# Kernel optimization log

Hardware: AMD Instinct MI355X
Metric: run time of the kernel (lower is better)

## Reference

```python
import jax, jax.numpy as jnp
import numpy as np

B, HRES, WRES, C, HEADS, WS, SS = 32, 64, 64, 256, 8, 8, 4
N = WS * WS
HID = 4 * C
EPS = 1e-5


def _rel_pos_index(ws):
    coords = np.stack(np.meshgrid(np.arange(ws), np.arange(ws), indexing='ij'))  # [2,ws,ws]
    cf = coords.reshape(2, -1)
    rel = (cf[:, :, None] - cf[:, None, :]).transpose(1, 2, 0)  # [N,N,2]
    rel[:, :, 0] += ws - 1
    rel[:, :, 1] += ws - 1
    rel[:, :, 0] *= 2 * ws - 1
    return rel.sum(-1).reshape(-1)  # [N*N]


def _attn_mask(H, W, ws, ss):
    img = np.zeros((H, W))
    cnt = 0
    for hs in (slice(0, -ws), slice(-ws, -ss), slice(-ss, None)):
        for wsl in (slice(0, -ws), slice(-ws, -ss), slice(-ss, None)):
            img[hs, wsl] = cnt
            cnt += 1
    mw = img.reshape(H // ws, ws, W // ws, ws).transpose(0, 2, 1, 3).reshape(-1, ws * ws)
    am = mw[:, None, :] - mw[:, :, None]  # [nW,N,N]
    return np.where(am != 0, -100.0, 0.0).astype(np.float32)


_RPI = jnp.asarray(_rel_pos_index(WS))
_MASK = jnp.asarray(_attn_mask(HRES, WRES, WS, SS))  # [nW,N,N]


def _ln(x, g, b):
    m = x.mean(-1, keepdims=True)
    v = ((x - m) ** 2).mean(-1, keepdims=True)
    return (x - m) / jnp.sqrt(v + EPS) * g + b


def setup_inputs() -> dict:
    key = jax.random.key(0)
    ks = jax.random.split(key, 16)
    s = 0.02
    return {
        'x': jax.random.normal(ks[0], (B, HRES * WRES, C), jnp.float32),
        'norm1_g': jnp.ones((C,), jnp.float32),
        'norm1_b': jnp.zeros((C,), jnp.float32),
        'qkv_w': jax.random.normal(ks[1], (3 * C, C), jnp.float32) * s,
        'qkv_b': jnp.zeros((3 * C,), jnp.float32),
        'rpb_table': jax.random.normal(ks[2], ((2 * WS - 1) ** 2, HEADS), jnp.float32) * s,
        'proj_w': jax.random.normal(ks[3], (C, C), jnp.float32) * s,
        'proj_b': jnp.zeros((C,), jnp.float32),
        'norm2_g': jnp.ones((C,), jnp.float32),
        'norm2_b': jnp.zeros((C,), jnp.float32),
        'fc1_w': jax.random.normal(ks[4], (HID, C), jnp.float32) * s,
        'fc1_b': jnp.zeros((HID,), jnp.float32),
        'fc2_w': jax.random.normal(ks[5], (C, HID), jnp.float32) * s,
        'fc2_b': jnp.zeros((C,), jnp.float32),
        'H': HRES,
        'W': WRES,
    }


def reference(x, norm1_g, norm1_b, qkv_w, qkv_b, rpb_table, proj_w, proj_b,
              norm2_g, norm2_b, fc1_w, fc1_b, fc2_w, fc2_b, H, W):
    Bn, L, Cd = x.shape
    ws, ss, nh = WS, SS, HEADS
    hd = Cd // nh
    shortcut = x
    h = _ln(x, norm1_g, norm1_b).reshape(Bn, H, W, Cd)
    # cyclic shift (H,W divisible by ws -> no padding needed)
    h = jnp.roll(h, (-ss, -ss), axis=(1, 2))
    # window partition: [B,H,W,C] -> [B*nW, N, C]
    h = h.reshape(Bn, H // ws, ws, W // ws, ws, Cd).transpose(0, 1, 3, 2, 4, 5).reshape(-1, N, Cd)
    qkv = (h @ qkv_w.T + qkv_b).reshape(-1, N, 3, nh, hd).transpose(2, 0, 3, 1, 4)
    q, k, v = qkv[0], qkv[1], qkv[2]  # [B_,h,N,d]
    attn = jnp.einsum('bhnd,bhmd->bhnm', q * (hd ** -0.5), k)
    rpb = rpb_table[_RPI].reshape(N, N, nh).transpose(2, 0, 1)  # [h,N,N]
    attn = attn + rpb[None]
    nW = _MASK.shape[0]
    attn = attn.reshape(Bn, nW, nh, N, N) + _MASK[None, :, None]
    attn = jax.nn.softmax(attn.reshape(-1, nh, N, N), axis=-1)
    o = jnp.einsum('bhnm,bhmd->bhnd', attn, v).transpose(0, 2, 1, 3).reshape(-1, N, Cd)
    o = o @ proj_w.T + proj_b
    # window reverse + reverse shift
    o = o.reshape(Bn, H // ws, W // ws, ws, ws, Cd).transpose(0, 1, 3, 2, 4, 5).reshape(Bn, H, W, Cd)
    o = jnp.roll(o, (ss, ss), axis=(1, 2)).reshape(Bn, L, Cd)
    x = shortcut + o
    h2 = _ln(x, norm2_g, norm2_b)
    h2 = jax.nn.gelu(h2 @ fc1_w.T + fc1_b, approximate=False)
    return x + (h2 @ fc2_w.T + fc2_b)
```

## Files before the change

kernel.cpp:

```cpp
#include <hip/hip_runtime.h>
#include <hip/hip_bf16.h>
#include <stdint.h>

typedef __bf16 bf16_t;
typedef __bf16 bf16x8 __attribute__((ext_vector_type(8)));
typedef __bf16 bf16x4 __attribute__((ext_vector_type(4)));
typedef float f32x4 __attribute__((ext_vector_type(4)));

#define MROWS 131072

__device__ __forceinline__ bf16_t to_bf16(float f) {
  __hip_bfloat16 h = __float2bfloat16(f);
  return *reinterpret_cast<bf16_t*>(&h);
}

__device__ __forceinline__ f32x4 mfma16(bf16x8 a, bf16x8 b, f32x4 c) {
  return __builtin_amdgcn_mfma_f32_16x16x32_bf16(a, b, c, 0, 0, 0);
}

__device__ __forceinline__ void gload16(const void* g, void* l) {
  __builtin_amdgcn_global_load_lds(
      (const __attribute__((address_space(1))) void*)g,
      (__attribute__((address_space(3))) void*)l, 16, 0, 0);
}

__device__ __forceinline__ int map_row(int m) {
  int b   = m >> 12;
  int rem = m & 4095;
  int win = rem >> 6;
  int n   = rem & 63;
  int gh  = ((win >> 3) << 3) + (n >> 3);
  int gw  = ((win & 7) << 3) + (n & 7);
  int sh  = (gh + 4) & 63;
  int sw  = (gw + 4) & 63;
  return (b << 12) + (sh << 6) + sw;
}

__global__ __launch_bounds__(256) void cvt_kernel(const float* __restrict__ in,
                                                  bf16_t* __restrict__ out, int n) {
  int i = blockIdx.x * 256 + threadIdx.x;
  if (i < n) out[i] = to_bf16(in[i]);
}

__global__ __launch_bounds__(256) void bias_kernel(const float* __restrict__ rpbt,
                                                   float* __restrict__ bias) {
  int idx = blockIdx.x * 256 + threadIdx.x;
  int m = idx & 63, n = (idx >> 6) & 63, h = (idx >> 12) & 7, c = idx >> 15;
  int yn = n >> 3, xn = n & 7, ym = m >> 3, xm = m & 7;
  float v = rpbt[((yn - ym + 7) * 15 + (xn - xm + 7)) * 8 + h];
  int rn = (c & 2) ? (yn < 4 ? 1 : 2) : 0;
  int cn = (c & 1) ? (xn < 4 ? 1 : 2) : 0;
  int rm = (c & 2) ? (ym < 4 ? 1 : 2) : 0;
  int cm = (c & 1) ? (xm < 4 ? 1 : 2) : 0;
  if (rn * 3 + cn != rm * 3 + cm) v -= 100.0f;
  bias[idx] = v;
}

template <bool PERM>
__global__ __launch_bounds__(256) void ln_kernel(const float* __restrict__ xin,
                                                 const float* __restrict__ g,
                                                 const float* __restrict__ b,
                                                 bf16_t* __restrict__ out) {
  int row  = (blockIdx.x << 2) + (threadIdx.x >> 6);
  int lane = threadIdx.x & 63;
  int src  = PERM ? map_row(row) : row;
  float4 v = *reinterpret_cast<const float4*>(xin + (size_t)src * 256 + (lane << 2));
  float s = v.x + v.y + v.z + v.w;
#pragma unroll
  for (int d = 1; d < 64; d <<= 1) s += __shfl_xor(s, d);
  float mean = s * 0.00390625f;
  float ax = v.x - mean, ay = v.y - mean, az = v.z - mean, aw = v.w - mean;
  float s2 = ax * ax + ay * ay + az * az + aw * aw;
#pragma unroll
  for (int d = 1; d < 64; d <<= 1) s2 += __shfl_xor(s2, d);
  float rstd = rsqrtf(s2 * 0.00390625f + 1e-5f);
  float4 gv = *reinterpret_cast<const float4*>(g + (lane << 2));
  float4 bv = *reinterpret_cast<const float4*>(b + (lane << 2));
  bf16x4 o4;
  o4[0] = to_bf16(ax * rstd * gv.x + bv.x);
  o4[1] = to_bf16(ay * rstd * gv.y + bv.y);
  o4[2] = to_bf16(az * rstd * gv.z + bv.z);
  o4[3] = to_bf16(aw * rstd * gv.w + bv.w);
  *reinterpret_cast<bf16x4*>(out + (size_t)row * 256 + (lane << 2)) = o4;
}

template <int EPI>
__global__ __launch_bounds__(256) void gemm_bt(const bf16_t* __restrict__ A,
                                               const bf16_t* __restrict__ W,
                                               const float* __restrict__ bias,
                                               void* __restrict__ outp,
                                               void* __restrict__ outp2,
                                               void* __restrict__ outp3,
                                               const float* __restrict__ resid,
                                               int M, int N, int K) {
  __shared__ __align__(16) bf16_t As[128 * 32];
  __shared__ __align__(16) bf16_t Bs[128 * 32];
  const int tid  = threadIdx.x;
  const int lane = tid & 63, lo = lane & 15, hi = lane >> 4;
  const int wave = tid >> 6;
  const int bm = blockIdx.x << 7, bn = blockIdx.y << 7;
  const int wr = (wave >> 1) << 6, wc = (wave & 1) << 6;
  f32x4 acc[4][4] = {};

  for (int k0 = 0; k0 < K; k0 += 32) {
    __syncthreads();
#pragma unroll
    for (int it = 0; it < 2; ++it) {
      int ch = (it << 8) + tid;
      int r = ch >> 2, kf = (ch & 3) << 3;
      gload16(A + (size_t)(bm + r) * K + (k0 + kf), &As[ch << 3]);
      gload16(W + (size_t)(bn + r) * K + (k0 + kf), &Bs[ch << 3]);
    }
    __syncthreads();
    bf16x8 af[4], bfr[4];
#pragma unroll
    for (int i = 0; i < 4; ++i)
      af[i] = *reinterpret_cast<const bf16x8*>(&As[(wr + (i << 4) + lo) * 32 + (hi << 3)]);
#pragma unroll
    for (int j = 0; j < 4; ++j)
      bfr[j] = *reinterpret_cast<const bf16x8*>(&Bs[(wc + (j << 4) + lo) * 32 + (hi << 3)]);
#pragma unroll
    for (int i = 0; i < 4; ++i)
#pragma unroll
      for (int j = 0; j < 4; ++j)
        acc[i][j] = mfma16(af[i], bfr[j], acc[i][j]);
  }

  float bv[4];
#pragma unroll
  for (int j = 0; j < 4; ++j) bv[j] = bias[bn + wc + (j << 4) + lo];

#pragma unroll
  for (int i = 0; i < 4; ++i) {
#pragma unroll
    for (int r = 0; r < 4; ++r) {
      int row = bm + wr + (i << 4) + (hi << 2) + r;
      if constexpr (EPI == 2) {
        int xr = map_row(row);
        float* o = (float*)outp;
#pragma unroll
        for (int j = 0; j < 4; ++j) {
          int col = bn + wc + (j << 4) + lo;
          size_t idx = (size_t)xr * 256 + col;
          o[idx] = resid[idx] + acc[i][j][r] + bv[j];
        }
      } else if constexpr (EPI == 3) {
        float* o = (float*)outp;
#pragma unroll
        for (int j = 0; j < 4; ++j) {
          int col = bn + wc + (j << 4) + lo;
          size_t idx = (size_t)row * 256 + col;
          o[idx] = o[idx] + acc[i][j][r] + bv[j];
        }
      } else if constexpr (EPI == 4) {
#pragma unroll
        for (int j = 0; j < 4; ++j) {
          int col = bn + wc + (j << 4) + lo;
          bf16_t* base = (col < 256) ? (bf16_t*)outp
                        : (col < 512) ? (bf16_t*)outp2 : (bf16_t*)outp3;
          int hd = (col >> 5) & 7, d = col & 31;
          base[((size_t)hd * MROWS + row) * 32 + d] = to_bf16(acc[i][j][r] + bv[j]);
        }
      } else {
        bf16_t* o = (bf16_t*)outp;
#pragma unroll
        for (int j = 0; j < 4; ++j) {
          int col = bn + wc + (j << 4) + lo;
          float v = acc[i][j][r] + bv[j];
          if constexpr (EPI == 1) v = 0.5f * v * (1.0f + erff(v * 0.70710678118654752f));
          o[(size_t)row * N + col] = to_bf16(v);
        }
      }
    }
  }
}

__global__ __launch_bounds__(256) void attn_kernel(const bf16_t* __restrict__ qh,
                                                   const bf16_t* __restrict__ kh,
                                                   const bf16_t* __restrict__ vh,
                                                   const float* __restrict__ bias,
                                                   bf16_t* __restrict__ o) {
  __shared__ __align__(16) bf16_t Pl[4][64 * 72];
  __shared__ __align__(16) bf16_t Vt[4][32 * 72];
  const int wave = threadIdx.x >> 6, lane = threadIdx.x & 63;
  const int lo = lane & 15, hi = lane >> 4;
  const int id = (blockIdx.x << 2) + wave;
  const int win = id >> 3, h = id & 7;
  const size_t hb = ((size_t)h * MROWS + (size_t)win * 64) * 32;
  const bf16_t* qb = qh + hb;
  const bf16_t* kb = kh + hb;
  const bf16_t* vb = vh + hb;

  const bf16_t* vbl = vb + lane * 32;
#pragma unroll
  for (int c4 = 0; c4 < 4; ++c4) {
    bf16x8 v8 = *reinterpret_cast<const bf16x8*>(vbl + (c4 << 3));
#pragma unroll
    for (int e = 0; e < 8; ++e) Vt[wave][((c4 << 3) + e) * 72 + lane] = v8[e];
  }

  bf16x8 qa[4], ka[4];
#pragma unroll
  for (int i = 0; i < 4; ++i)
    qa[i] = *reinterpret_cast<const bf16x8*>(qb + ((i << 4) + lo) * 32 + (hi << 3));
#pragma unroll
  for (int j = 0; j < 4; ++j)
    ka[j] = *reinterpret_cast<const bf16x8*>(kb + ((j << 4) + lo) * 32 + (hi << 3));
  f32x4 s[4][4] = {};
#pragma unroll
  for (int i = 0; i < 4; ++i)
#pragma unroll
    for (int j = 0; j < 4; ++j) s[i][j] = mfma16(qa[i], ka[j], s[i][j]);

  const int wh = (win & 63) >> 3, ww = win & 7;
  const int cls = ((wh == 7) ? 2 : 0) + ((ww == 7) ? 1 : 0);
  const float* bb = bias + ((size_t)cls * 8 + h) * 4096;
  const float scale = 0.17677669529663687f;

  float pinv[4][4];
#pragma unroll
  for (int i = 0; i < 4; ++i) {
#pragma unroll
    for (int r = 0; r < 4; ++r) {
      int n = (i << 4) + (hi << 2) + r;
      const float* brow = bb + n * 64 + lo;
      float vals[4], mx = -1e30f;
#pragma unroll
      for (int j = 0; j < 4; ++j) {
        float val = s[i][j][r] * scale + brow[j << 4];
        vals[j] = val;
        mx = fmaxf(mx, val);
      }
#pragma unroll
      for (int d = 1; d < 16; d <<= 1) mx = fmaxf(mx, __shfl_xor(mx, d));
      float sum = 0.0f;
#pragma unroll
      for (int j = 0; j < 4; ++j) {
        float p = __expf(vals[j] - mx);
        sum += p;
        Pl[wave][n * 72 + (j << 4) + lo] = to_bf16(p);
      }
#pragma unroll
      for (int d = 1; d < 16; d <<= 1) sum += __shfl_xor(sum, d);
      pinv[i][r] = 1.0f / sum;
    }
  }

  __syncthreads();

  f32x4 oa[4][2] = {};
#pragma unroll
  for (int kt = 0; kt < 2; ++kt) {
    bf16x8 pa[4], va[2];
#pragma unroll
    for (int i = 0; i < 4; ++i)
      pa[i] = *reinterpret_cast<const bf16x8*>(&Pl[wave][((i << 4) + lo) * 72 + (kt << 5) + (hi << 3)]);
#pragma unroll
    for (int dt = 0; dt < 2; ++dt)
      va[dt] = *reinterpret_cast<const bf16x8*>(&Vt[wave][((dt << 4) + lo) * 72 + (kt << 5) + (hi << 3)]);
#pragma unroll
    for (int i = 0; i < 4; ++i)
#pragma unroll
      for (int dt = 0; dt < 2; ++dt) oa[i][dt] = mfma16(pa[i], va[dt], oa[i][dt]);
  }

  bf16_t* ob = o + (size_t)win * (64 * 256) + h * 32;
#pragma unroll
  for (int i = 0; i < 4; ++i)
#pragma unroll
    for (int r = 0; r < 4; ++r) {
      int n = (i << 4) + (hi << 2) + r;
      float piv = pinv[i][r];
#pragma unroll
      for (int dt = 0; dt < 2; ++dt)
        ob[(size_t)n * 256 + (dt << 4) + lo] = to_bf16(oa[i][dt][r] * piv);
    }
}

extern "C" void kernel_launch(void* const* d_in, const int* in_sizes, int n_in,
                              void* d_out, int out_size, void* d_ws, size_t ws_size,
                              hipStream_t stream) {
  const float* x      = (const float*)d_in[0];
  const float* n1g    = (const float*)d_in[1];
  const float* n1b    = (const float*)d_in[2];
  const float* qkv_w  = (const float*)d_in[3];
  const float* qkv_b  = (const float*)d_in[4];
  const float* rpbt   = (const float*)d_in[5];
  const float* proj_w = (const float*)d_in[6];
  const float* proj_b = (const float*)d_in[7];
  const float* n2g    = (const float*)d_in[8];
  const float* n2b    = (const float*)d_in[9];
  const float* fc1_w  = (const float*)d_in[10];
  const float* fc1_b  = (const float*)d_in[11];
  const float* fc2_w  = (const float*)d_in[12];
  const float* fc2_b  = (const float*)d_in[13];
  float* out = (float*)d_out;
  char*  ws  = (char*)d_ws;

  const size_t MB64 = 67108864;
  bf16_t* hln  = (bf16_t*)(ws);
  bf16_t* obuf = (bf16_t*)(ws);
  bf16_t* h2   = (bf16_t*)(ws);
  bf16_t* qbuf = (bf16_t*)(ws + MB64);
  bf16_t* x2n  = (bf16_t*)(ws + MB64);
  bf16_t* wb   = (bf16_t*)(ws + 2 * MB64);
  bf16_t* qkv_wb  = wb;
  bf16_t* proj_wb = qkv_wb + 196608;
  bf16_t* fc1_wb  = proj_wb + 65536;
  bf16_t* fc2_wb  = fc1_wb + 262144;
  float*  biast   = (float*)(fc2_wb + 262144);
  bf16_t* kbuf = (bf16_t*)d_out;
  bf16_t* vbuf = kbuf + 33554432;

  cvt_kernel<<<768, 256, 0, stream>>>(qkv_w, qkv_wb, 196608);
  cvt_kernel<<<256, 256, 0, stream>>>(proj_w, proj_wb, 65536);
  cvt_kernel<<<1024, 256, 0, stream>>>(fc1_w, fc1_wb, 262144);
  cvt_kernel<<<1024, 256, 0, stream>>>(fc2_w, fc2_wb, 262144);
  bias_kernel<<<512, 256, 0, stream>>>(rpbt, biast);

  ln_kernel<true><<<32768, 256, 0, stream>>>(x, n1g, n1b, hln);

  gemm_bt<4><<<dim3(1024, 6), 256, 0, stream>>>(hln, qkv_wb, qkv_b, qbuf, kbuf, vbuf,
                                                nullptr, MROWS, 768, 256);

  attn_kernel<<<4096, 256, 0, stream>>>(qbuf, kbuf, vbuf, biast, obuf);

  gemm_bt<2><<<dim3(1024, 2), 256, 0, stream>>>(obuf, proj_wb, proj_b, out, nullptr, nullptr,
                                                x, MROWS, 256, 256);

  ln_kernel<false><<<32768, 256, 0, stream>>>(out, n2g, n2b, x2n);

  for (int c = 0; c < 4; ++c) {
    const bf16_t* xa = x2n + (size_t)c * 32768 * 256;
    gemm_bt<1><<<dim3(256, 8), 256, 0, stream>>>(xa, fc1_wb, fc1_b, h2, nullptr, nullptr,
                                                 nullptr, 32768, 1024, 256);
    gemm_bt<3><<<dim3(256, 2), 256, 0, stream>>>(h2, fc2_wb, fc2_b, out + (size_t)c * 32768 * 256,
                                                 nullptr, nullptr, nullptr, 32768, 256, 1024);
  }
}
```

Measured before the change: 681.4 us.

## Fuse LN1, QKV projection, window attention and output projection into one kernel

Replaces the separate LN1, QKV GEMM, attention and proj GEMM kernels with a single per-window kernel. Each block takes one window, with one wave per head, and keeps the normalized rows, q/k/v and the attention output in LDS. This removes the round trips of the intermediate QKV and attention-output tensors through global memory. Weights are now read straight from global memory per wave without LDS tiling, and the large LDS footprint limits occupancy. The MLP GEMM grid is also swapped so blockIdx.x walks the N tiles.

Result: faster. 644.4 us (-5.4%).

```diff
diff --git a/kernel.cpp b/kernel.cpp
--- a/kernel.cpp
+++ b/kernel.cpp
@@ -4,7 +4,6 @@
 
 typedef __bf16 bf16_t;
 typedef __bf16 bf16x8 __attribute__((ext_vector_type(8)));
-typedef __bf16 bf16x4 __attribute__((ext_vector_type(4)));
 typedef float f32x4 __attribute__((ext_vector_type(4)));
 
 #define MROWS 131072
@@ -56,15 +55,13 @@
   bias[idx] = v;
 }
 
-template <bool PERM>
 __global__ __launch_bounds__(256) void ln_kernel(const float* __restrict__ xin,
                                                  const float* __restrict__ g,
                                                  const float* __restrict__ b,
                                                  bf16_t* __restrict__ out) {
   int row  = (blockIdx.x << 2) + (threadIdx.x >> 6);
   int lane = threadIdx.x & 63;
-  int src  = PERM ? map_row(row) : row;
-  float4 v = *reinterpret_cast<const float4*>(xin + (size_t)src * 256 + (lane << 2));
+  float4 v = *reinterpret_cast<const float4*>(xin + (size_t)row * 256 + (lane << 2));
   float s = v.x + v.y + v.z + v.w;
 #pragma unroll
   for (int d = 1; d < 64; d <<= 1) s += __shfl_xor(s, d);
@@ -76,6 +73,7 @@
   float rstd = rsqrtf(s2 * 0.00390625f + 1e-5f);
   float4 gv = *reinterpret_cast<const float4*>(g + (lane << 2));
   float4 bv = *reinterpret_cast<const float4*>(b + (lane << 2));
+  typedef __bf16 bf16x4 __attribute__((ext_vector_type(4)));
   bf16x4 o4;
   o4[0] = to_bf16(ax * rstd * gv.x + bv.x);
   o4[1] = to_bf16(ay * rstd * gv.y + bv.y);
@@ -89,16 +87,13 @@
                                                const bf16_t* __restrict__ W,
                                                const float* __restrict__ bias,
                                                void* __restrict__ outp,
-                                               void* __restrict__ outp2,
-                                               void* __restrict__ outp3,
-                                               const float* __restrict__ resid,
                                                int M, int N, int K) {
   __shared__ __align__(16) bf16_t As[128 * 32];
   __shared__ __align__(16) bf16_t Bs[128 * 32];
   const int tid  = threadIdx.x;
   const int lane = tid & 63, lo = lane & 15, hi = lane >> 4;
   const int wave = tid >> 6;
-  const int bm = blockIdx.x << 7, bn = blockIdx.y << 7;
+  const int bm = blockIdx.y << 7, bn = blockIdx.x << 7;
   const int wr = (wave >> 1) << 6, wc = (wave & 1) << 6;
   f32x4 acc[4][4] = {};
 
@@ -135,31 +130,13 @@
 #pragma unroll
     for (int r = 0; r < 4; ++r) {
       int row = bm + wr + (i << 4) + (hi << 2) + r;
-      if constexpr (EPI == 2) {
-        int xr = map_row(row);
-        float* o = (float*)outp;
-#pragma unroll
-        for (int j = 0; j < 4; ++j) {
-          int col = bn + wc + (j << 4) + lo;
-          size_t idx = (size_t)xr * 256 + col;
-          o[idx] = resid[idx] + acc[i][j][r] + bv[j];
-        }
-      } else if constexpr (EPI == 3) {
+      if constexpr (EPI == 3) {
         float* o = (float*)outp;
 #pragma unroll
         for (int j = 0; j < 4; ++j) {
           int col = bn + wc + (j << 4) + lo;
           size_t idx = (size_t)row * 256 + col;
           o[idx] = o[idx] + acc[i][j][r] + bv[j];
-        }
-      } else if constexpr (EPI == 4) {
-#pragma unroll
-        for (int j = 0; j < 4; ++j) {
-          int col = bn + wc + (j << 4) + lo;
-          bf16_t* base = (col < 256) ? (bf16_t*)outp
-                        : (col < 512) ? (bf16_t*)outp2 : (bf16_t*)outp3;
-          int hd = (col >> 5) & 7, d = col & 31;
-          base[((size_t)hd * MROWS + row) * 32 + d] = to_bf16(acc[i][j][r] + bv[j]);
         }
       } else {
         bf16_t* o = (bf16_t*)outp;
@@ -175,42 +152,117 @@
   }
 }
 
-__global__ __launch_bounds__(256) void attn_kernel(const bf16_t* __restrict__ qh,
-                                                   const bf16_t* __restrict__ kh,
-                                                   const bf16_t* __restrict__ vh,
-                                                   const float* __restrict__ bias,
-                                                   bf16_t* __restrict__ o) {
-  __shared__ __align__(16) bf16_t Pl[4][64 * 72];
-  __shared__ __align__(16) bf16_t Vt[4][32 * 72];
-  const int wave = threadIdx.x >> 6, lane = threadIdx.x & 63;
-  const int lo = lane & 15, hi = lane >> 4;
-  const int id = (blockIdx.x << 2) + wave;
-  const int win = id >> 3, h = id & 7;
-  const size_t hb = ((size_t)h * MROWS + (size_t)win * 64) * 32;
-  const bf16_t* qb = qh + hb;
-  const bf16_t* kb = kh + hb;
-  const bf16_t* vb = vh + hb;
-
-  const bf16_t* vbl = vb + lane * 32;
-#pragma unroll
-  for (int c4 = 0; c4 < 4; ++c4) {
-    bf16x8 v8 = *reinterpret_cast<const bf16x8*>(vbl + (c4 << 3));
-#pragma unroll
-    for (int e = 0; e < 8; ++e) Vt[wave][((c4 << 3) + e) * 72 + lane] = v8[e];
-  }
+__global__ __launch_bounds__(512, 2) void mega_attn(
+    const float* __restrict__ x, const float* __restrict__ n1g,
+    const float* __restrict__ n1b, const bf16_t* __restrict__ qkv_wb,
+    const float* __restrict__ qkv_b, const bf16_t* __restrict__ proj_wb,
+    const float* __restrict__ proj_b, const float* __restrict__ bias,
+    float* __restrict__ out) {
+  extern __shared__ __align__(16) char smem_raw[];
+  bf16_t* Sm = (bf16_t*)smem_raw;
+  bf16_t* A_lds = Sm;
+  const int tid = threadIdx.x;
+  const int lane = tid & 63, lo = lane & 15, hi = lane >> 4;
+  const int h = tid >> 6;
+  const int win = blockIdx.x;
+  bf16_t* Wv    = Sm + 16896 + h * 7424;
+  bf16_t* q_lds = Wv;
+  bf16_t* k_lds = Wv + 2560;
+  bf16_t* Vt    = Wv + 5120;
+  bf16_t* Pl    = Wv;
+
+  {
+    const int row = tid >> 3, s = tid & 7;
+    const int src = map_row((win << 6) + row);
+    const float* xp = x + (size_t)src * 256 + (s << 5);
+    float f[32];
+#pragma unroll
+    for (int c = 0; c < 8; ++c) {
+      float4 v = *reinterpret_cast<const float4*>(xp + (c << 2));
+      f[c * 4 + 0] = v.x; f[c * 4 + 1] = v.y; f[c * 4 + 2] = v.z; f[c * 4 + 3] = v.w;
+    }
+    float sum = 0.0f;
+#pragma unroll
+    for (int e = 0; e < 32; ++e) sum += f[e];
+#pragma unroll
+    for (int d = 1; d < 8; d <<= 1) sum += __shfl_xor(sum, d);
+    float mean = sum * 0.00390625f;
+    float var = 0.0f;
+#pragma unroll
+    for (int e = 0; e < 32; ++e) { float t = f[e] - mean; var += t * t; }
+#pragma unroll
+    for (int d = 1; d < 8; d <<= 1) var += __shfl_xor(var, d);
+    float rstd = rsqrtf(var * 0.00390625f + 1e-5f);
+    const float* gp = n1g + (s << 5);
+    const float* bp = n1b + (s << 5);
+#pragma unroll
+    for (int c = 0; c < 4; ++c) {
+      bf16x8 w;
+#pragma unroll
+      for (int e = 0; e < 8; ++e) {
+        int idx = (c << 3) + e;
+        w[e] = to_bf16((f[idx] - mean) * rstd * gp[idx] + bp[idx]);
+      }
+      *reinterpret_cast<bf16x8*>(&A_lds[row * 264 + (s << 5) + (c << 3)]) = w;
+    }
+  }
+  __syncthreads();
+
+  f32x4 aq[2][4] = {}, ak[2][4] = {}, av[2][4] = {};
+#pragma unroll 2
+  for (int kk = 0; kk < 8; ++kk) {
+    const int k0 = kk << 5;
+    bf16x8 fb[4];
+#pragma unroll
+    for (int j = 0; j < 4; ++j)
+      fb[j] = *reinterpret_cast<const bf16x8*>(&A_lds[((j << 4) + lo) * 264 + k0 + (hi << 3)]);
+    bf16x8 wfq[2], wfk[2], wfv[2];
+#pragma unroll
+    for (int i = 0; i < 2; ++i) {
+      int drow = h * 32 + (i << 4) + lo;
+      wfq[i] = *reinterpret_cast<const bf16x8*>(qkv_wb + (size_t)(drow      ) * 256 + k0 + (hi << 3));
+      wfk[i] = *reinterpret_cast<const bf16x8*>(qkv_wb + (size_t)(drow + 256) * 256 + k0 + (hi << 3));
+      wfv[i] = *reinterpret_cast<const bf16x8*>(qkv_wb + (size_t)(drow + 512) * 256 + k0 + (hi << 3));
+    }
+#pragma unroll
+    for (int i = 0; i < 2; ++i)
+#pragma unroll
+      for (int j = 0; j < 4; ++j) {
+        aq[i][j] = mfma16(wfq[i], fb[j], aq[i][j]);
+        ak[i][j] = mfma16(wfk[i], fb[j], ak[i][j]);
+        av[i][j] = mfma16(wfv[i], fb[j], av[i][j]);
+      }
+  }
+
+#pragma unroll
+  for (int i = 0; i < 2; ++i)
+#pragma unroll
+    for (int r = 0; r < 4; ++r) {
+      int d = (i << 4) + (hi << 2) + r;
+      float bq = qkv_b[h * 32 + d];
+      float bk = qkv_b[256 + h * 32 + d];
+      float bv = qkv_b[512 + h * 32 + d];
+#pragma unroll
+      for (int j = 0; j < 4; ++j) {
+        int n = (j << 4) + lo;
+        q_lds[n * 40 + d] = to_bf16(aq[i][j][r] + bq);
+        k_lds[n * 40 + d] = to_bf16(ak[i][j][r] + bk);
+        Vt[d * 72 + n]    = to_bf16(av[i][j][r] + bv);
+      }
+    }
 
   bf16x8 qa[4], ka[4];
 #pragma unroll
   for (int i = 0; i < 4; ++i)
-    qa[i] = *reinterpret_cast<const bf16x8*>(qb + ((i << 4) + lo) * 32 + (hi << 3));
+    qa[i] = *reinterpret_cast<const bf16x8*>(&q_lds[((i << 4) + lo) * 40 + (hi << 3)]);
 #pragma unroll
   for (int j = 0; j < 4; ++j)
-    ka[j] = *reinterpret_cast<const bf16x8*>(kb + ((j << 4) + lo) * 32 + (hi << 3));
-  f32x4 s[4][4] = {};
+    ka[j] = *reinterpret_cast<const bf16x8*>(&k_lds[((j << 4) + lo) * 40 + (hi << 3)]);
+  f32x4 s4[4][4] = {};
 #pragma unroll
   for (int i = 0; i < 4; ++i)
 #pragma unroll
-    for (int j = 0; j < 4; ++j) s[i][j] = mfma16(qa[i], ka[j], s[i][j]);
+    for (int j = 0; j < 4; ++j) s4[i][j] = mfma16(qa[i], ka[j], s4[i][j]);
 
   const int wh = (win & 63) >> 3, ww = win & 7;
   const int cls = ((wh == 7) ? 2 : 0) + ((ww == 7) ? 1 : 0);
@@ -227,7 +279,7 @@
       float vals[4], mx = -1e30f;
 #pragma unroll
       for (int j = 0; j < 4; ++j) {
-        float val = s[i][j][r] * scale + brow[j << 4];
+        float val = s4[i][j][r] * scale + brow[j << 4];
         vals[j] = val;
         mx = fmaxf(mx, val);
       }
@@ -238,7 +290,7 @@
       for (int j = 0; j < 4; ++j) {
         float p = __expf(vals[j] - mx);
         sum += p;
-        Pl[wave][n * 72 + (j << 4) + lo] = to_bf16(p);
+        Pl[n * 72 + (j << 4) + lo] = to_bf16(p);
       }
 #pragma unroll
       for (int d = 1; d < 16; d <<= 1) sum += __shfl_xor(sum, d);
@@ -246,25 +298,23 @@
     }
   }
 
-  __syncthreads();
-
   f32x4 oa[4][2] = {};
 #pragma unroll
   for (int kt = 0; kt < 2; ++kt) {
     bf16x8 pa[4], va[2];
 #pragma unroll
     for (int i = 0; i < 4; ++i)
-      pa[i] = *reinterpret_cast<const bf16x8*>(&Pl[wave][((i << 4) + lo) * 72 + (kt << 5) + (hi << 3)]);
+      pa[i] = *reinterpret_cast<const bf16x8*>(&Pl[((i << 4) + lo) * 72 + (kt << 5) + (hi << 3)]);
 #pragma unroll
     for (int dt = 0; dt < 2; ++dt)
-      va[dt] = *reinterpret_cast<const bf16x8*>(&Vt[wave][((dt << 4) + lo) * 72 + (kt << 5) + (hi << 3)]);
+      va[dt] = *reinterpret_cast<const bf16x8*>(&Vt[((dt << 4) + lo) * 72 + (kt << 5) + (hi << 3)]);
 #pragma unroll
     for (int i = 0; i < 4; ++i)
 #pragma unroll
       for (int dt = 0; dt < 2; ++dt) oa[i][dt] = mfma16(pa[i], va[dt], oa[i][dt]);
   }
 
-  bf16_t* ob = o + (size_t)win * (64 * 256) + h * 32;
+  __syncthreads();
 #pragma unroll
   for (int i = 0; i < 4; ++i)
 #pragma unroll
@@ -273,7 +323,39 @@
       float piv = pinv[i][r];
 #pragma unroll
       for (int dt = 0; dt < 2; ++dt)
-        ob[(size_t)n * 256 + (dt << 4) + lo] = to_bf16(oa[i][dt][r] * piv);
+        A_lds[n * 264 + h * 32 + (dt << 4) + lo] = to_bf16(oa[i][dt][r] * piv);
+    }
+  __syncthreads();
+
+  f32x4 ap[4][2] = {};
+#pragma unroll 2
+  for (int kk = 0; kk < 8; ++kk) {
+    const int k0 = kk << 5;
+    bf16x8 fa[4], wp[2];
+#pragma unroll
+    for (int i = 0; i < 4; ++i)
+      fa[i] = *reinterpret_cast<const bf16x8*>(&A_lds[((i << 4) + lo) * 264 + k0 + (hi << 3)]);
+#pragma unroll
+    for (int jj = 0; jj < 2; ++jj)
+      wp[jj] = *reinterpret_cast<const bf16x8*>(proj_wb + (size_t)(h * 32 + (jj << 4) + lo) * 256 + k0 + (hi << 3));
+#pragma unroll
+    for (int i = 0; i < 4; ++i)
+#pragma unroll
+      for (int jj = 0; jj < 2; ++jj)
+        ap[i][jj] = mfma16(fa[i], wp[jj], ap[i][jj]);
+  }
+#pragma unroll
+  for (int i = 0; i < 4; ++i)
+#pragma unroll
+    for (int r = 0; r < 4; ++r) {
+      int m = (i << 4) + (hi << 2) + r;
+      int xr = map_row((win << 6) + m);
+#pragma unroll
+      for (int jj = 0; jj < 2; ++jj) {
+        int col = h * 32 + (jj << 4) + lo;
+        size_t idx = (size_t)xr * 256 + col;
+        out[idx] = x[idx] + ap[i][jj][r] + proj_b[col];
+      }
     }
 }
 
@@ -298,10 +380,7 @@
   char*  ws  = (char*)d_ws;
 
   const size_t MB64 = 67108864;
-  bf16_t* hln  = (bf16_t*)(ws);
-  bf16_t* obuf = (bf16_t*)(ws);
   bf16_t* h2   = (bf16_t*)(ws);
-  bf16_t* qbuf = (bf16_t*)(ws + MB64);
   bf16_t* x2n  = (bf16_t*)(ws + MB64);
   bf16_t* wb   = (bf16_t*)(ws + 2 * MB64);
   bf16_t* qkv_wb  = wb;
@@ -309,8 +388,10 @@
   bf16_t* fc1_wb  = proj_wb + 65536;
   bf16_t* fc2_wb  = fc1_wb + 262144;
   float*  biast   = (float*)(fc2_wb + 262144);
-  bf16_t* kbuf = (bf16_t*)d_out;
-  bf16_t* vbuf = kbuf + 33554432;
+
+  static const int MEGA_LDS = 152576;
+  hipFuncSetAttribute(reinterpret_cast<const void*>(mega_attn),
+                      hipFuncAttributeMaxDynamicSharedMemorySize, MEGA_LDS);
 
   cvt_kernel<<<768, 256, 0, stream>>>(qkv_w, qkv_wb, 196608);
   cvt_kernel<<<256, 256, 0, stream>>>(proj_w, proj_wb, 65536);
@@ -318,23 +399,15 @@
   cvt_kernel<<<1024, 256, 0, stream>>>(fc2_w, fc2_wb, 262144);
   bias_kernel<<<512, 256, 0, stream>>>(rpbt, biast);
 
-  ln_kernel<true><<<32768, 256, 0, stream>>>(x, n1g, n1b, hln);
-
-  gemm_bt<4><<<dim3(1024, 6), 256, 0, stream>>>(hln, qkv_wb, qkv_b, qbuf, kbuf, vbuf,
-                                                nullptr, MROWS, 768, 256);
-
-  attn_kernel<<<4096, 256, 0, stream>>>(qbuf, kbuf, vbuf, biast, obuf);
-
-  gemm_bt<2><<<dim3(1024, 2), 256, 0, stream>>>(obuf, proj_wb, proj_b, out, nullptr, nullptr,
-                                                x, MROWS, 256, 256);
-
-  ln_kernel<false><<<32768, 256, 0, stream>>>(out, n2g, n2b, x2n);
+  mega_attn<<<2048, 512, MEGA_LDS, stream>>>(x, n1g, n1b, qkv_wb, qkv_b,
+                                             proj_wb, proj_b, biast, out);
+
+  ln_kernel<<<32768, 256, 0, stream>>>(out, n2g, n2b, x2n);
 
   for (int c = 0; c < 4; ++c) {
     const bf16_t* xa = x2n + (size_t)c * 32768 * 256;
-    gemm_bt<1><<<dim3(256, 8), 256, 0, stream>>>(xa, fc1_wb, fc1_b, h2, nullptr, nullptr,
-                                                 nullptr, 32768, 1024, 256);
-    gemm_bt<3><<<dim3(256, 2), 256, 0, stream>>>(h2, fc2_wb, fc2_b, out + (size_t)c * 32768 * 256,
-                                                 nullptr, nullptr, nullptr, 32768, 256, 1024);
-  }
-}
+    gemm_bt<1><<<dim3(8, 256), 256, 0, stream>>>(xa, fc1_wb, fc1_b, h2, 32768, 1024, 256);
+    gemm_bt<3><<<dim3(2, 256), 256, 0, stream>>>(h2, fc2_wb, fc2_b, out + (size_t)c * 32768 * 256,
+                                                 32768, 256, 1024);
+  }
+}
```

## Fuse MLP fc1-GELU-fc2 into one kernel and keep QKV A-tile resident

Applied to the files above, without the earlier changes.

Replaces the four-chunk fc1/fc2 GEMM pair with one fused MLP kernel. Each block holds a 64-row activation tile in swizzled LDS, computes 256-wide chunks of the hidden layer with GELU into LDS, and accumulates fc2 directly, so the 1024-wide hidden tensor never goes to global memory. The QKV GEMM now loads its full 128x256 A tile into LDS once and loops over all 768 output columns, so A is not re-read for each N tile. Weights in both kernels are read straight from global memory without LDS staging. This relies on cache hits for the weights, and the larger LDS use lowers occupancy.

Measured after the change: 1.169 ms. 71.5% more time.

```diff
diff --git a/kernel.cpp b/kernel.cpp
--- a/kernel.cpp
+++ b/kernel.cpp
@@ -84,92 +84,69 @@
   *reinterpret_cast<bf16x4*>(out + (size_t)row * 256 + (lane << 2)) = o4;
 }
 
-template <int EPI>
-__global__ __launch_bounds__(256) void gemm_bt(const bf16_t* __restrict__ A,
-                                               const bf16_t* __restrict__ W,
-                                               const float* __restrict__ bias,
-                                               void* __restrict__ outp,
-                                               void* __restrict__ outp2,
-                                               void* __restrict__ outp3,
-                                               const float* __restrict__ resid,
-                                               int M, int N, int K) {
-  __shared__ __align__(16) bf16_t As[128 * 32];
-  __shared__ __align__(16) bf16_t Bs[128 * 32];
-  const int tid  = threadIdx.x;
+__global__ __launch_bounds__(256) void qkv_ares(const bf16_t* __restrict__ A,
+                                                const bf16_t* __restrict__ W,
+                                                const float* __restrict__ bias,
+                                                bf16_t* __restrict__ q,
+                                                bf16_t* __restrict__ k,
+                                                bf16_t* __restrict__ v) {
+  extern __shared__ __align__(16) char smem_raw[];
+  bf16_t* As = (bf16_t*)smem_raw;
+  const int tid = threadIdx.x;
   const int lane = tid & 63, lo = lane & 15, hi = lane >> 4;
   const int wave = tid >> 6;
-  const int bm = blockIdx.x << 7, bn = blockIdx.y << 7;
+  const int bm = blockIdx.x << 7;
   const int wr = (wave >> 1) << 6, wc = (wave & 1) << 6;
-  f32x4 acc[4][4] = {};
-
-  for (int k0 = 0; k0 < K; k0 += 32) {
-    __syncthreads();
-#pragma unroll
-    for (int it = 0; it < 2; ++it) {
-      int ch = (it << 8) + tid;
-      int r = ch >> 2, kf = (ch & 3) << 3;
-      gload16(A + (size_t)(bm + r) * K + (k0 + kf), &As[ch << 3]);
-      gload16(W + (size_t)(bn + r) * K + (k0 + kf), &Bs[ch << 3]);
-    }
-    __syncthreads();
-    bf16x8 af[4], bfr[4];
-#pragma unroll
-    for (int i = 0; i < 4; ++i)
-      af[i] = *reinterpret_cast<const bf16x8*>(&As[(wr + (i << 4) + lo) * 32 + (hi << 3)]);
-#pragma unroll
-    for (int j = 0; j < 4; ++j)
-      bfr[j] = *reinterpret_cast<const bf16x8*>(&Bs[(wc + (j << 4) + lo) * 32 + (hi << 3)]);
-#pragma unroll
-    for (int i = 0; i < 4; ++i)
-#pragma unroll
-      for (int j = 0; j < 4; ++j)
-        acc[i][j] = mfma16(af[i], bfr[j], acc[i][j]);
-  }
-
-  float bv[4];
-#pragma unroll
-  for (int j = 0; j < 4; ++j) bv[j] = bias[bn + wc + (j << 4) + lo];
-
-#pragma unroll
-  for (int i = 0; i < 4; ++i) {
-#pragma unroll
-    for (int r = 0; r < 4; ++r) {
-      int row = bm + wr + (i << 4) + (hi << 2) + r;
-      if constexpr (EPI == 2) {
-        int xr = map_row(row);
-        float* o = (float*)outp;
-#pragma unroll
-        for (int j = 0; j < 4; ++j) {
-          int col = bn + wc + (j << 4) + lo;
-          size_t idx = (size_t)xr * 256 + col;
-          o[idx] = resid[idx] + acc[i][j][r] + bv[j];
-        }
-      } else if constexpr (EPI == 3) {
-        float* o = (float*)outp;
-#pragma unroll
-        for (int j = 0; j < 4; ++j) {
-          int col = bn + wc + (j << 4) + lo;
-          size_t idx = (size_t)row * 256 + col;
-          o[idx] = o[idx] + acc[i][j][r] + bv[j];
-        }
-      } else if constexpr (EPI == 4) {
-#pragma unroll
-        for (int j = 0; j < 4; ++j) {
-          int col = bn + wc + (j << 4) + lo;
-          bf16_t* base = (col < 256) ? (bf16_t*)outp
-                        : (col < 512) ? (bf16_t*)outp2 : (bf16_t*)outp3;
-          int hd = (col >> 5) & 7, d = col & 31;
-          base[((size_t)hd * MROWS + row) * 32 + d] = to_bf16(acc[i][j][r] + bv[j]);
-        }
-      } else {
-        bf16_t* o = (bf16_t*)outp;
-#pragma unroll
-        for (int j = 0; j < 4; ++j) {
-          int col = bn + wc + (j << 4) + lo;
-          float v = acc[i][j][r] + bv[j];
-          if constexpr (EPI == 1) v = 0.5f * v * (1.0f + erff(v * 0.70710678118654752f));
-          o[(size_t)row * N + col] = to_bf16(v);
-        }
+
+#pragma unroll
+  for (int it = 0; it < 16; ++it) {
+    int c = (it << 8) + tid;
+    int g = c ^ ((c >> 5) & 7);
+    gload16(A + (size_t)(bm + (c >> 5)) * 256 + ((g & 31) << 3), &As[c << 3]);
+  }
+  __syncthreads();
+
+  for (int nbp = 0; nbp < 3; ++nbp) {
+    f32x4 acc[2][4][4] = {};
+    for (int kk = 0; kk < 8; ++kk) {
+      bf16x8 af[4];
+#pragma unroll
+      for (int i = 0; i < 4; ++i) {
+        int row = wr + (i << 4) + lo;
+        af[i] = *reinterpret_cast<const bf16x8*>(
+            &As[row * 256 + ((((kk << 2) + hi) ^ (row & 7)) << 3)]);
+      }
+#pragma unroll
+      for (int half = 0; half < 2; ++half) {
+        int bn = (nbp << 8) + (half << 7);
+        bf16x8 wf[4];
+#pragma unroll
+        for (int j = 0; j < 4; ++j)
+          wf[j] = *reinterpret_cast<const bf16x8*>(
+              W + (size_t)(bn + wc + (j << 4) + lo) * 256 + (kk << 5) + (hi << 3));
+#pragma unroll
+        for (int i = 0; i < 4; ++i)
+#pragma unroll
+          for (int j = 0; j < 4; ++j)
+            acc[half][i][j] = mfma16(af[i], wf[j], acc[half][i][j]);
+      }
+    }
+#pragma unroll
+    for (int half = 0; half < 2; ++half) {
+      int bn = (nbp << 8) + (half << 7);
+#pragma unroll
+      for (int j = 0; j < 4; ++j) {
+        int col = bn + wc + (j << 4) + lo;
+        float bv = bias[col];
+        bf16_t* base = (col < 256) ? q : (col < 512) ? k : v;
+        int hd = (col >> 5) & 7, d = col & 31;
+#pragma unroll
+        for (int i = 0; i < 4; ++i)
+#pragma unroll
+          for (int r = 0; r < 4; ++r) {
+            int row = bm + wr + (i << 4) + (hi << 2) + r;
+            base[((size_t)hd * MROWS + row) * 32 + d] = to_bf16(acc[half][i][j][r] + bv);
+          }
       }
     }
   }
@@ -275,6 +252,151 @@
       for (int dt = 0; dt < 2; ++dt)
         ob[(size_t)n * 256 + (dt << 4) + lo] = to_bf16(oa[i][dt][r] * piv);
     }
+}
+
+__global__ __launch_bounds__(256) void gemm_proj(const bf16_t* __restrict__ A,
+                                                 const bf16_t* __restrict__ W,
+                                                 const float* __restrict__ bias,
+                                                 float* __restrict__ out,
+                                                 const float* __restrict__ resid) {
+  __shared__ __align__(16) bf16_t As[128 * 32];
+  __shared__ __align__(16) bf16_t Bs[128 * 32];
+  const int tid  = threadIdx.x;
+  const int lane = tid & 63, lo = lane & 15, hi = lane >> 4;
+  const int wave = tid >> 6;
+  const int bm = blockIdx.x << 7, bn = blockIdx.y << 7;
+  const int wr = (wave >> 1) << 6, wc = (wave & 1) << 6;
+  f32x4 acc[4][4] = {};
+
+  for (int k0 = 0; k0 < 256; k0 += 32) {
+    __syncthreads();
+#pragma unroll
+    for (int it = 0; it < 2; ++it) {
+      int ch = (it << 8) + tid;
+      int r = ch >> 2, kf = (ch & 3) << 3;
+      gload16(A + (size_t)(bm + r) * 256 + (k0 + kf), &As[ch << 3]);
+      gload16(W + (size_t)(bn + r) * 256 + (k0 + kf), &Bs[ch << 3]);
+    }
+    __syncthreads();
+    bf16x8 af[4], bfr[4];
+#pragma unroll
+    for (int i = 0; i < 4; ++i)
+      af[i] = *reinterpret_cast<const bf16x8*>(&As[(wr + (i << 4) + lo) * 32 + (hi << 3)]);
+#pragma unroll
+    for (int j = 0; j < 4; ++j)
+      bfr[j] = *reinterpret_cast<const bf16x8*>(&Bs[(wc + (j << 4) + lo) * 32 + (hi << 3)]);
+#pragma unroll
+    for (int i = 0; i < 4; ++i)
+#pragma unroll
+      for (int j = 0; j < 4; ++j)
+        acc[i][j] = mfma16(af[i], bfr[j], acc[i][j]);
+  }
+
+  float bv[4];
+#pragma unroll
+  for (int j = 0; j < 4; ++j) bv[j] = bias[bn + wc + (j << 4) + lo];
+
+#pragma unroll
+  for (int i = 0; i < 4; ++i)
+#pragma unroll
+    for (int r = 0; r < 4; ++r) {
+      int row = bm + wr + (i << 4) + (hi << 2) + r;
+      int xr = map_row(row);
+#pragma unroll
+      for (int j = 0; j < 4; ++j) {
+        int col = bn + wc + (j << 4) + lo;
+        size_t idx = (size_t)xr * 256 + col;
+        out[idx] = resid[idx] + acc[i][j][r] + bv[j];
+      }
+    }
+}
+
+__global__ __launch_bounds__(256) void mlp_fused(const bf16_t* __restrict__ A,
+                                                 const bf16_t* __restrict__ W1,
+                                                 const float* __restrict__ b1,
+                                                 const bf16_t* __restrict__ W2,
+                                                 const float* __restrict__ b2,
+                                                 float* __restrict__ out) {
+  extern __shared__ __align__(16) char smem_raw[];
+  bf16_t* As = (bf16_t*)smem_raw;
+  bf16_t* Hs = As + 16384;
+  const int tid = threadIdx.x;
+  const int lane = tid & 63, lo = lane & 15, hi = lane >> 4;
+  const int wave = tid >> 6;
+  const int bm = blockIdx.x << 6;
+  const int wr = (wave >> 1) << 5;
+  const int wc = (wave & 1) << 7;
+
+#pragma unroll
+  for (int it = 0; it < 8; ++it) {
+    int c = (it << 8) + tid;
+    int g = c ^ ((c >> 5) & 7);
+    gload16(A + (size_t)(bm + (c >> 5)) * 256 + ((g & 31) << 3), &As[c << 3]);
+  }
+  __syncthreads();
+
+  f32x4 acc2[2][8] = {};
+  for (int nc = 0; nc < 4; ++nc) {
+    f32x4 acc1[2][8] = {};
+    for (int kk = 0; kk < 8; ++kk) {
+      bf16x8 af[2];
+#pragma unroll
+      for (int i = 0; i < 2; ++i) {
+        int row = wr + (i << 4) + lo;
+        af[i] = *reinterpret_cast<const bf16x8*>(
+            &As[row * 256 + ((((kk << 2) + hi) ^ (row & 7)) << 3)]);
+      }
+#pragma unroll
+      for (int j = 0; j < 8; ++j) {
+        bf16x8 wf = *reinterpret_cast<const bf16x8*>(
+            W1 + (size_t)((nc << 8) + wc + (j << 4) + lo) * 256 + (kk << 5) + (hi << 3));
+#pragma unroll
+        for (int i = 0; i < 2; ++i) acc1[i][j] = mfma16(af[i], wf, acc1[i][j]);
+      }
+    }
+#pragma unroll
+    for (int j = 0; j < 8; ++j) {
+      float bb = b1[(nc << 8) + wc + (j << 4) + lo];
+#pragma unroll
+      for (int i = 0; i < 2; ++i)
+#pragma unroll
+        for (int r = 0; r < 4; ++r) {
+          int row = wr + (i << 4) + (hi << 2) + r;
+          float vv = acc1[i][j][r] + bb;
+          vv = 0.5f * vv * (1.0f + erff(vv * 0.70710678118654752f));
+          Hs[row * 264 + wc + (j << 4) + lo] = to_bf16(vv);
+        }
+    }
+    __syncthreads();
+    for (int kk = 0; kk < 8; ++kk) {
+      bf16x8 hf[2];
+#pragma unroll
+      for (int i = 0; i < 2; ++i)
+        hf[i] = *reinterpret_cast<const bf16x8*>(
+            &Hs[(wr + (i << 4) + lo) * 264 + (kk << 5) + (hi << 3)]);
+#pragma unroll
+      for (int j = 0; j < 8; ++j) {
+        bf16x8 wf = *reinterpret_cast<const bf16x8*>(
+            W2 + (size_t)(wc + (j << 4) + lo) * 1024 + (nc << 8) + (kk << 5) + (hi << 3));
+#pragma unroll
+        for (int i = 0; i < 2; ++i) acc2[i][j] = mfma16(hf[i], wf, acc2[i][j]);
+      }
+    }
+    __syncthreads();
+  }
+
+#pragma unroll
+  for (int j = 0; j < 8; ++j) {
+    float bb = b2[wc + (j << 4) + lo];
+#pragma unroll
+    for (int i = 0; i < 2; ++i)
+#pragma unroll
+      for (int r = 0; r < 4; ++r) {
+        int row = bm + wr + (i << 4) + (hi << 2) + r;
+        size_t idx = (size_t)row * 256 + wc + (j << 4) + lo;
+        out[idx] = out[idx] + acc2[i][j][r] + bb;
+      }
+  }
 }
 
 extern "C" void kernel_launch(void* const* d_in, const int* in_sizes, int n_in,
@@ -300,7 +422,6 @@
   const size_t MB64 = 67108864;
   bf16_t* hln  = (bf16_t*)(ws);
   bf16_t* obuf = (bf16_t*)(ws);
-  bf16_t* h2   = (bf16_t*)(ws);
   bf16_t* qbuf = (bf16_t*)(ws + MB64);
   bf16_t* x2n  = (bf16_t*)(ws + MB64);
   bf16_t* wb   = (bf16_t*)(ws + 2 * MB64);
@@ -312,6 +433,11 @@
   bf16_t* kbuf = (bf16_t*)d_out;
   bf16_t* vbuf = kbuf + 33554432;
 
+  hipFuncSetAttribute(reinterpret_cast<const void*>(qkv_ares),
+                      hipFuncAttributeMaxDynamicSharedMemorySize, 65536);
+  hipFuncSetAttribute(reinterpret_cast<const void*>(mlp_fused),
+                      hipFuncAttributeMaxDynamicSharedMemorySize, 66560);
+
   cvt_kernel<<<768, 256, 0, stream>>>(qkv_w, qkv_wb, 196608);
   cvt_kernel<<<256, 256, 0, stream>>>(proj_w, proj_wb, 65536);
   cvt_kernel<<<1024, 256, 0, stream>>>(fc1_w, fc1_wb, 262144);
@@ -320,21 +446,13 @@
 
   ln_kernel<true><<<32768, 256, 0, stream>>>(x, n1g, n1b, hln);
 
-  gemm_bt<4><<<dim3(1024, 6), 256, 0, stream>>>(hln, qkv_wb, qkv_b, qbuf, kbuf, vbuf,
-                                                nullptr, MROWS, 768, 256);
+  qkv_ares<<<1024, 256, 65536, stream>>>(hln, qkv_wb, qkv_b, qbuf, kbuf, vbuf);
 
   attn_kernel<<<4096, 256, 0, stream>>>(qbuf, kbuf, vbuf, biast, obuf);
 
-  gemm_bt<2><<<dim3(1024, 2), 256, 0, stream>>>(obuf, proj_wb, proj_b, out, nullptr, nullptr,
-                                                x, MROWS, 256, 256);
+  gemm_proj<<<dim3(1024, 2), 256, 0, stream>>>(obuf, proj_wb, proj_b, out, x);
 
   ln_kernel<false><<<32768, 256, 0, stream>>>(out, n2g, n2b, x2n);
 
-  for (int c = 0; c < 4; ++c) {
-    const bf16_t* xa = x2n + (size_t)c * 32768 * 256;
-    gemm_bt<1><<<dim3(256, 8), 256, 0, stream>>>(xa, fc1_wb, fc1_b, h2, nullptr, nullptr,
-                                                 nullptr, 32768, 1024, 256);
-    gemm_bt<3><<<dim3(256, 2), 256, 0, stream>>>(h2, fc2_wb, fc2_b, out + (size_t)c * 32768 * 256,
-                                                 nullptr, nullptr, nullptr, 32768, 256, 1024);
-  }
-}
+  mlp_fused<<<2048, 256, 66560, stream>>>(x2n, fc1_wb, fc1_b, fc2_wb, fc2_b, out);
+}
```

## Double-buffer GEMM LDS tiles, remap blocks for XCD-local N reuse, fuse weight conversions

Applied to the files above, without the earlier changes.

The GEMM now keeps two LDS buffers and issues global-to-LDS loads for the next K tile while MFMAs run on the current one, dropping one barrier per iteration. The 2D grid becomes a 1D grid whose block index is permuted so consecutive workgroups on the same XCD share an A row-tile across all N tiles, which is meant to improve L2 reuse. The four weight-conversion launches are merged into one kernel. In exchange, LDS per block doubles, which can lower occupancy.

Result: faster. 668.0 us (-2.0%).

```diff
diff --git a/kernel.cpp b/kernel.cpp
--- a/kernel.cpp
+++ b/kernel.cpp
@@ -36,10 +36,19 @@
   return (b << 12) + (sh << 6) + sw;
 }
 
-__global__ __launch_bounds__(256) void cvt_kernel(const float* __restrict__ in,
-                                                  bf16_t* __restrict__ out, int n) {
+__global__ __launch_bounds__(256) void cvt_all(const float* __restrict__ qkv_w,
+                                               const float* __restrict__ proj_w,
+                                               const float* __restrict__ fc1_w,
+                                               const float* __restrict__ fc2_w,
+                                               bf16_t* __restrict__ qkv_o,
+                                               bf16_t* __restrict__ proj_o,
+                                               bf16_t* __restrict__ fc1_o,
+                                               bf16_t* __restrict__ fc2_o) {
   int i = blockIdx.x * 256 + threadIdx.x;
-  if (i < n) out[i] = to_bf16(in[i]);
+  if (i < 196608)       qkv_o[i] = to_bf16(qkv_w[i]);
+  else if (i < 262144)  proj_o[i - 196608] = to_bf16(proj_w[i - 196608]);
+  else if (i < 524288)  fc1_o[i - 262144] = to_bf16(fc1_w[i - 262144]);
+  else                  fc2_o[i - 524288] = to_bf16(fc2_w[i - 524288]);
 }
 
 __global__ __launch_bounds__(256) void bias_kernel(const float* __restrict__ rpbt,
@@ -92,39 +101,51 @@
                                                void* __restrict__ outp2,
                                                void* __restrict__ outp3,
                                                const float* __restrict__ resid,
-                                               int M, int N, int K) {
-  __shared__ __align__(16) bf16_t As[128 * 32];
-  __shared__ __align__(16) bf16_t Bs[128 * 32];
+                                               int M, int N, int K, int NBN) {
+  __shared__ __align__(16) bf16_t As[2][128 * 32];
+  __shared__ __align__(16) bf16_t Bs[2][128 * 32];
   const int tid  = threadIdx.x;
   const int lane = tid & 63, lo = lane & 15, hi = lane >> 4;
   const int wave = tid >> 6;
-  const int bm = blockIdx.x << 7, bn = blockIdx.y << 7;
+  const int cpx = gridDim.x >> 3;
+  const int wg  = (blockIdx.x & 7) * cpx + (blockIdx.x >> 3);
+  const int bn = (wg % NBN) << 7, bm = (wg / NBN) << 7;
   const int wr = (wave >> 1) << 6, wc = (wave & 1) << 6;
   f32x4 acc[4][4] = {};
 
-  for (int k0 = 0; k0 < K; k0 += 32) {
-    __syncthreads();
-#pragma unroll
-    for (int it = 0; it < 2; ++it) {
-      int ch = (it << 8) + tid;
-      int r = ch >> 2, kf = (ch & 3) << 3;
-      gload16(A + (size_t)(bm + r) * K + (k0 + kf), &As[ch << 3]);
-      gload16(W + (size_t)(bn + r) * K + (k0 + kf), &Bs[ch << 3]);
-    }
-    __syncthreads();
+#define STAGE(buf, kt)                                                     \
+  {                                                                        \
+    int k0s = (kt) << 5;                                                   \
+    _Pragma("unroll") for (int it = 0; it < 2; ++it) {                     \
+      int ch = (it << 8) + tid;                                            \
+      int r = ch >> 2, kf = (ch & 3) << 3;                                 \
+      gload16(A + (size_t)(bm + r) * K + k0s + kf, &As[buf][ch << 3]);     \
+      gload16(W + (size_t)(bn + r) * K + k0s + kf, &Bs[buf][ch << 3]);     \
+    }                                                                      \
+  }
+
+  const int nt = K >> 5;
+  STAGE(0, 0);
+  __syncthreads();
+
+  for (int t = 0; t < nt; ++t) {
+    const int cur = t & 1;
+    if (t + 1 < nt) STAGE(cur ^ 1, t + 1);
     bf16x8 af[4], bfr[4];
 #pragma unroll
     for (int i = 0; i < 4; ++i)
-      af[i] = *reinterpret_cast<const bf16x8*>(&As[(wr + (i << 4) + lo) * 32 + (hi << 3)]);
+      af[i] = *reinterpret_cast<const bf16x8*>(&As[cur][(wr + (i << 4) + lo) * 32 + (hi << 3)]);
 #pragma unroll
     for (int j = 0; j < 4; ++j)
-      bfr[j] = *reinterpret_cast<const bf16x8*>(&Bs[(wc + (j << 4) + lo) * 32 + (hi << 3)]);
+      bfr[j] = *reinterpret_cast<const bf16x8*>(&Bs[cur][(wc + (j << 4) + lo) * 32 + (hi << 3)]);
 #pragma unroll
     for (int i = 0; i < 4; ++i)
 #pragma unroll
       for (int j = 0; j < 4; ++j)
         acc[i][j] = mfma16(af[i], bfr[j], acc[i][j]);
-  }
+    __syncthreads();
+  }
+#undef STAGE
 
   float bv[4];
 #pragma unroll
@@ -312,29 +333,27 @@
   bf16_t* kbuf = (bf16_t*)d_out;
   bf16_t* vbuf = kbuf + 33554432;
 
-  cvt_kernel<<<768, 256, 0, stream>>>(qkv_w, qkv_wb, 196608);
-  cvt_kernel<<<256, 256, 0, stream>>>(proj_w, proj_wb, 65536);
-  cvt_kernel<<<1024, 256, 0, stream>>>(fc1_w, fc1_wb, 262144);
-  cvt_kernel<<<1024, 256, 0, stream>>>(fc2_w, fc2_wb, 262144);
+  cvt_all<<<3072, 256, 0, stream>>>(qkv_w, proj_w, fc1_w, fc2_w,
+                                    qkv_wb, proj_wb, fc1_wb, fc2_wb);
   bias_kernel<<<512, 256, 0, stream>>>(rpbt, biast);
 
   ln_kernel<true><<<32768, 256, 0, stream>>>(x, n1g, n1b, hln);
 
-  gemm_bt<4><<<dim3(1024, 6), 256, 0, stream>>>(hln, qkv_wb, qkv_b, qbuf, kbuf, vbuf,
-                                                nullptr, MROWS, 768, 256);
+  gemm_bt<4><<<6144, 256, 0, stream>>>(hln, qkv_wb, qkv_b, qbuf, kbuf, vbuf,
+                                       nullptr, MROWS, 768, 256, 6);
 
   attn_kernel<<<4096, 256, 0, stream>>>(qbuf, kbuf, vbuf, biast, obuf);
 
-  gemm_bt<2><<<dim3(1024, 2), 256, 0, stream>>>(obuf, proj_wb, proj_b, out, nullptr, nullptr,
-                                                x, MROWS, 256, 256);
+  gemm_bt<2><<<2048, 256, 0, stream>>>(obuf, proj_wb, proj_b, out, nullptr, nullptr,
+                                       x, MROWS, 256, 256, 2);
 
   ln_kernel<false><<<32768, 256, 0, stream>>>(out, n2g, n2b, x2n);
 
   for (int c = 0; c < 4; ++c) {
     const bf16_t* xa = x2n + (size_t)c * 32768 * 256;
-    gemm_bt<1><<<dim3(256, 8), 256, 0, stream>>>(xa, fc1_wb, fc1_b, h2, nullptr, nullptr,
-                                                 nullptr, 32768, 1024, 256);
-    gemm_bt<3><<<dim3(256, 2), 256, 0, stream>>>(h2, fc2_wb, fc2_b, out + (size_t)c * 32768 * 256,
-                                                 nullptr, nullptr, nullptr, 32768, 256, 1024);
-  }
-}
+    gemm_bt<1><<<2048, 256, 0, stream>>>(xa, fc1_wb, fc1_b, h2, nullptr, nullptr,
+                                         nullptr, 32768, 1024, 256, 8);
+    gemm_bt<3><<<512, 256, 0, stream>>>(h2, fc2_wb, fc2_b, out + (size_t)c * 32768 * 256,
+                                        nullptr, nullptr, nullptr, 32768, 256, 1024, 2);
+  }
+}
```
